# Performance work log

Measured on AMD Instinct MI355X. Metric: run time of the kernel, lower is better.

## Reference

```python
import jax, jax.numpy as jnp
import numpy as np

N, E, O, C, D_IN, OUT, L, B = 10000, 80000, 10, 64, 16, 16, 2, 16
DEG, WIDEN, BD = 3, 4, 64
EPS = 1e-6


def fibonacci_sphere(n):
    # deterministic near-uniform grid of n unit vectors on S^2 (stands in for GridGenerator's repulsion grid)
    i = jnp.arange(n, dtype=jnp.float32) + 0.5
    phi = jnp.arccos(1.0 - 2.0 * i / n)
    theta = jnp.pi * (1.0 + 5.0 ** 0.5) * i
    return jnp.stack([jnp.cos(theta) * jnp.sin(phi), jnp.sin(theta) * jnp.sin(phi), jnp.cos(phi)], axis=-1)


def poly_features(x, degree):
    # PolynomialFeatures: concat x, x(x)x, x(x)x(x)x, ... flattened outer products
    feats = [x]
    cur = x
    for _ in range(degree):
        cur = (cur[..., :, None] * x[..., None, :]).reshape(x.shape[:-1] + (-1,))
        feats.append(cur)
    return jnp.concatenate(feats, axis=-1)


def layer_norm(x, scale, bias):
    mu = jnp.mean(x, axis=-1, keepdims=True)
    var = jnp.mean((x - mu) ** 2, axis=-1, keepdims=True)
    return (x - mu) * jax.lax.rsqrt(var + EPS) * scale + bias


def setup_inputs():
    key = jax.random.key(0)
    ks = jax.random.split(key, 16)
    def w(k, shape):
        return jax.random.normal(k, shape, dtype=jnp.float32) / np.sqrt(shape[-2])
    P_SP = 2 + 4 + 8 + 16  # poly features of 2-dim spatial invariants, degree 3
    P_OR = 4               # poly features of 1-dim orientation invariant, degree 3
    return {
        "x": jax.random.normal(ks[0], (N, D_IN), jnp.float32),
        "pos": jax.random.normal(ks[1], (N, 3), jnp.float32),
        "basis_w1": w(ks[2], (P_SP, C)), "basis_b1": jnp.zeros((C,), jnp.float32),
        "basis_w2": w(ks[3], (C, BD)), "basis_b2": jnp.zeros((BD,), jnp.float32),
        "fbasis_w1": w(ks[4], (P_OR, C)), "fbasis_b1": jnp.zeros((C,), jnp.float32),
        "fbasis_w2": w(ks[5], (C, BD)), "fbasis_b2": jnp.zeros((BD,), jnp.float32),
        "embed_w": w(ks[6], (D_IN, C)),
        "conv_kw": w(ks[7], (L, BD, C)),
        "conv_fw": w(ks[8], (L, BD, C)),
        "conv_b": jnp.zeros((L, C), jnp.float32),
        "norm_s": jnp.ones((L, C), jnp.float32),
        "norm_b": jnp.zeros((L, C), jnp.float32),
        "lin1_w": w(ks[9], (L, C, WIDEN * C)), "lin1_b": jnp.zeros((L, WIDEN * C), jnp.float32),
        "lin2_w": w(ks[10], (L, WIDEN * C, C)), "lin2_b": jnp.zeros((L, C), jnp.float32),
        "ro_w": w(ks[11], (L, C, OUT)), "ro_b": jnp.zeros((L, OUT), jnp.float32),
        "edge_index": jax.random.randint(ks[12], (2, E), 0, N, jnp.int32),
        "batch": jnp.sort(jax.random.randint(ks[13], (N,), 0, B, jnp.int32)),
    }


def reference(x, pos, basis_w1, basis_b1, basis_w2, basis_b2, fbasis_w1, fbasis_b1, fbasis_w2, fbasis_b2, embed_w, conv_kw, conv_fw, conv_b, norm_s, norm_b, lin1_w, lin1_b, lin2_w, lin2_b, ro_w, ro_b, edge_index, batch):
    ori = fibonacci_sphere(O)                                             # [O,3]
    send, recv = edge_index[0], edge_index[1]
    rel = (pos[send] - pos[recv])[:, None, :]                              # [E,1,3]
    inv1 = jnp.sum(rel * ori[None], axis=-1, keepdims=True)                # [E,O,1]
    inv2 = jnp.linalg.norm(rel - inv1 * ori[None], axis=-1, keepdims=True) # [E,O,1]
    inv3 = jnp.sum(ori[None, :, :] * ori[:, None, :], axis=-1, keepdims=True)  # [O,O,1]
    sp = jnp.concatenate([inv1, inv2], axis=-1)                            # [E,O,2]
    kb = jax.nn.gelu(poly_features(sp, DEG) @ basis_w1 + basis_b1)
    kb = jax.nn.gelu(kb @ basis_w2 + basis_b2)                             # [E,O,BD]
    fkb = jax.nn.gelu(poly_features(inv3, DEG) @ fbasis_w1 + fbasis_b1)
    fkb = jax.nn.gelu(fkb @ fbasis_w2 + fbasis_b2)                         # [O,O,BD]
    h = jnp.broadcast_to((x @ embed_w)[:, None, :], (N, O, C))             # [N,O,C]
    readout = jnp.zeros((N, O, OUT), h.dtype)
    for l in range(L):
        # depthwise spatial conv: gather-send, modulate by kernel, scatter-add to receivers
        msg = h[send] * (kb @ conv_kw[l])                                  # [E,O,C]
        h1 = jax.ops.segment_sum(msg, recv, num_segments=N)                # [N,O,C]
        # depthwise fiber (orientation) conv
        fk = fkb @ conv_fw[l]                                              # [O,O,C]
        h2 = jnp.einsum('noc,poc->npc', h1, fk) / O + conv_b[l]
        # ConvNeXt MLP + residual
        y = layer_norm(h2, norm_s[l], norm_b[l])
        y = jax.nn.gelu(y @ lin1_w[l] + lin1_b[l]) @ lin2_w[l] + lin2_b[l]
        h = h + y
        readout = readout + (h @ ro_w[l] + ro_b[l])
    readout = readout / L
    out_scalar = jnp.mean(readout, axis=-2)                                # [N,OUT]
    pooled = jnp.zeros((B, OUT), out_scalar.dtype).at[batch].add(out_scalar)
    return pooled
```

## Files before the change

kernel.cpp:

```cpp
#include <hip/hip_runtime.h>
#include <math.h>

#define N_   10000
#define E_   80000
#define O_   10
#define B_   16
#define OUT_ 16
#define NROW_ (N_*O_)
#define NITEM_ (E_*O_)

typedef __attribute__((ext_vector_type(8))) short bf16x8;
typedef __attribute__((ext_vector_type(4))) short bf16x4;
typedef __attribute__((ext_vector_type(4))) float f32x4;

#define MFMA16(a,b,c) __builtin_amdgcn_mfma_f32_16x16x32_bf16(a,b,c,0,0,0)

__device__ __forceinline__ float gelu_f(float x) {
    float u = fmaf(0.044715f, x * x, 1.0f);
    float e = __builtin_amdgcn_exp2f(2.3022083f * x * u);
    float r = __builtin_amdgcn_rcpf(e + 1.0f);
    return fmaf(-x, r, x);
}

__device__ __forceinline__ unsigned short f2bf(float f) {
    union { float f; unsigned int u; } v; v.f = f;
    unsigned int r = v.u + 0x7FFFu + ((v.u >> 16) & 1u);
    return (unsigned short)(r >> 16);
}
__device__ __forceinline__ float bf2f(unsigned short u) {
    union { unsigned int u; float f; } v; v.u = ((unsigned int)u) << 16;
    return v.f;
}
__device__ __forceinline__ unsigned int cvtpk(float lo, float hi) {
    unsigned int r;
    asm("v_cvt_pk_bf16_f32 %0, %1, %2" : "=v"(r) : "v"(lo), "v"(hi));
    return r;
}
__device__ __forceinline__ bf16x4 pack4(float a, float b, float c, float d) {
    union { unsigned int u[2]; bf16x4 v; } z;
    z.u[0] = cvtpk(a, b);
    z.u[1] = cvtpk(c, d);
    return z.v;
}

__global__ __launch_bounds__(256) void k_small(
    const float* __restrict__ bw1,
    const float* __restrict__ fw1, const float* __restrict__ fb1,
    const float* __restrict__ fw2, const float* __restrict__ fb2,
    const float* __restrict__ cfw,
    const float* __restrict__ bw2, const float* __restrict__ ckw,
    const float* __restrict__ l1w, const float* __restrict__ l2w,
    const float* __restrict__ row_w,
    float* __restrict__ orig, float* __restrict__ fkg,
    unsigned short* __restrict__ wW1P, unsigned short* __restrict__ wW2P,
    unsigned short* __restrict__ wCKP, unsigned short* __restrict__ wL1P,
    unsigned short* __restrict__ wL2P, unsigned short* __restrict__ wROP)
{
    __shared__ float sOri[32];
    __shared__ float sHid[6400];
    __shared__ float sFkb[6400];
    __shared__ float sW1f[14*64];
    int tid = threadIdx.x;
    if (tid < O_) {
        float i = (float)tid + 0.5f;
        float phi = acosf(1.0f - 2.0f * i / (float)O_);
        float theta = 3.14159265358979323846f * (1.0f + 2.2360679774997896964f) * i;
        float sp = sinf(phi);
        float v0 = cosf(theta) * sp, v1 = sinf(theta) * sp, v2 = cosf(phi);
        sOri[tid*3+0] = v0; sOri[tid*3+1] = v1; sOri[tid*3+2] = v2;
        orig[tid*3+0] = v0; orig[tid*3+1] = v1; orig[tid*3+2] = v2;
    }
    {
        const int map[30] = {0,1, 2,3,3,4, 5,6,6,7,6,7,7,8,
                             9,10,10,11,10,11,11,12, 10,11,11,12, 11,12,12,13};
        for (int idx = tid; idx < 14*64; idx += 256) {
            int mono = idx >> 6, c = idx & 63;
            float s = 0.0f;
            for (int p = 0; p < 30; ++p) if (map[p] == mono) s += bw1[p*64 + c];
            sW1f[idx] = s;
        }
    }
    __syncthreads();
    for (int idx = tid; idx < 4*512; idx += 256) {
        int t = idx >> 9, rem = idx & 511;
        int ln = rem >> 3, j = rem & 7;
        int row = t*16 + (ln & 15);
        int k = (ln >> 4)*8 + j;
        wW1P[idx] = f2bf(k < 14 ? sW1f[k*64 + row] : 0.0f);
    }
    for (int idx = tid; idx < 8*512; idx += 256) {
        int t = idx >> 9, rem = idx & 511;
        int mt = t >> 1, ks = t & 1;
        int ln = rem >> 3, j = rem & 7;
        int row = mt*16 + (ln & 15);
        int k = ks*32 + (ln >> 4)*8 + j;
        wW2P[idx] = f2bf(bw2[k*64 + row]);
    }
    for (int idx = tid; idx < 2*8*512; idx += 256) {
        int l = idx >> 12, r2 = idx & 4095;
        int t = r2 >> 9, rem = r2 & 511;
        int mt = t >> 1, ks = t & 1;
        int ln = rem >> 3, j = rem & 7;
        int row = mt*16 + (ln & 15);
        int k = ks*32 + (ln >> 4)*8 + j;
        wCKP[idx] = f2bf(ckw[l*4096 + k*64 + row]);
    }
    for (int idx = tid; idx < 2*32*512; idx += 256) {
        int l = idx >> 14, r2 = idx & 16383;
        int t = r2 >> 9, rem = r2 & 511;
        int mt = t >> 1, ks = t & 1;
        int ln = rem >> 3, j = rem & 7;
        int row = mt*16 + (ln & 15);
        int k = ks*32 + (ln >> 4)*8 + j;
        wL1P[idx] = f2bf(l1w[l*16384 + k*256 + row]);
    }
    for (int idx = tid; idx < 2*32*512; idx += 256) {
        int l = idx >> 14, r2 = idx & 16383;
        int t = r2 >> 9, rem = r2 & 511;
        int mt2 = t >> 3, ksg = t & 7;
        int ln = rem >> 3, j = rem & 7;
        int row = mt2*16 + (ln & 15);
        int k = ksg*32 + (ln >> 4)*8 + j;
        wL2P[idx] = f2bf(l2w[l*16384 + k*64 + row]);
    }
    for (int idx = tid; idx < 2*2*512; idx += 256) {
        int l = idx >> 10, r2 = idx & 1023;
        int ks = r2 >> 9, rem = r2 & 511;
        int ln = rem >> 3, j = rem & 7;
        int row = ln & 15;
        int k = ks*32 + (ln >> 4)*8 + j;
        wROP[idx] = f2bf(row_w[l*1024 + k*16 + row]);
    }
    for (int it = tid; it < 6400; it += 256) {
        int pr = it >> 6, c = it & 63;
        int i = pr / O_, j = pr % O_;
        float a = sOri[i*3+0]*sOri[j*3+0] + sOri[i*3+1]*sOri[j*3+1] + sOri[i*3+2]*sOri[j*3+2];
        float f1 = a, f2 = a*a, f3 = f2*a, f4 = f3*a;
        float v = fb1[c];
        v = fmaf(f1, fw1[0*64+c], v);
        v = fmaf(f2, fw1[1*64+c], v);
        v = fmaf(f3, fw1[2*64+c], v);
        v = fmaf(f4, fw1[3*64+c], v);
        sHid[it] = gelu_f(v);
    }
    __syncthreads();
    for (int it = tid; it < 6400; it += 256) {
        int pr = it >> 6, c = it & 63;
        float v = fb2[c];
        for (int b = 0; b < 64; ++b) v = fmaf(sHid[pr*64+b], fw2[b*64+c], v);
        sFkb[it] = gelu_f(v);
    }
    __syncthreads();
    for (int l = 0; l < 2; ++l)
        for (int it = tid; it < 6400; it += 256) {
            int pr = it >> 6, c = it & 63;
            float v = 0.0f;
            for (int b = 0; b < 64; ++b) v = fmaf(sFkb[pr*64+b], cfw[l*4096 + b*64 + c], v);
            fkg[l*6400 + it] = v;
        }
}

__global__ __launch_bounds__(256) void k_embed(
    const float* __restrict__ x, const float* __restrict__ ew,
    float* __restrict__ hg, unsigned short* __restrict__ hbf0)
{
    int t = blockIdx.x * 256 + threadIdx.x;
    if (t >= N_ * 64) return;
    int n = t >> 6, c = t & 63;
    float v = 0.0f;
#pragma unroll
    for (int k = 0; k < 16; ++k) v = fmaf(x[n*16+k], ew[k*64+c], v);
    int base = n * 640 + c;
#pragma unroll
    for (int o = 0; o < O_; ++o) hg[base + o*64] = v;
    hbf0[t] = f2bf(v);
}

__global__ __launch_bounds__(256) void k_hist(const int* __restrict__ ei, int* __restrict__ counts)
{
    int e = blockIdx.x * 256 + threadIdx.x;
    if (e < E_) atomicAdd(&counts[ei[E_ + e]], 1);
}

__global__ __launch_bounds__(1024) void k_scan(
    const int* __restrict__ counts, int* __restrict__ offs, int* __restrict__ cursor)
{
    __shared__ int part[1024];
    int t = threadIdx.x;
    const int CH = 10;
    int base_i = t * CH;
    int s = 0;
#pragma unroll
    for (int i = 0; i < CH; ++i) { int idx = base_i + i; if (idx < N_) s += counts[idx]; }
    part[t] = s;
    __syncthreads();
    for (int off = 1; off < 1024; off <<= 1) {
        int v = (t >= off) ? part[t - off] : 0;
        __syncthreads();
        part[t] += v;
        __syncthreads();
    }
    int run = (t > 0) ? part[t - 1] : 0;
#pragma unroll
    for (int i = 0; i < CH; ++i) {
        int idx = base_i + i;
        if (idx < N_) { offs[idx] = run; cursor[idx] = run; run += counts[idx]; }
    }
    if (t == 1023) offs[N_] = run;
}

__global__ __launch_bounds__(256) void k_scatter(
    const int* __restrict__ ei, const float* __restrict__ pos,
    int* __restrict__ cursor, int* __restrict__ csend, int* __restrict__ crecv,
    float* __restrict__ crel)
{
    int e = blockIdx.x * 256 + threadIdx.x;
    if (e >= E_) return;
    int s = ei[e], r = ei[E_ + e];
    int slot = atomicAdd(&cursor[r], 1);
    csend[slot] = s;
    crecv[slot] = r;
    crel[slot*3+0] = pos[s*3+0] - pos[r*3+0];
    crel[slot*3+1] = pos[s*3+1] - pos[r*3+1];
    crel[slot*3+2] = pos[s*3+2] - pos[r*3+2];
}

template<int KS, bool BIAS, bool GELU>
__device__ __forceinline__ void mfma_stageP(
    unsigned short* sData, const unsigned short* __restrict__ Wp,
    const float* __restrict__ bias, int rbase, int lane)
{
    const int lm = lane & 15, lk = lane >> 4;
    bf16x8 Bf[4][KS];
#pragma unroll
    for (int nt = 0; nt < 4; ++nt)
#pragma unroll
        for (int ks = 0; ks < KS; ++ks) {
            int r = rbase + nt*16 + lm;
            int kb = ks*64 + lk*16;
            Bf[nt][ks] = *(const bf16x8*)((const char*)sData + r*128 + (kb ^ ((r&7)<<4)));
        }
#pragma unroll
    for (int mt = 0; mt < 4; ++mt) {
        bf16x8 Af[KS];
#pragma unroll
        for (int ks = 0; ks < KS; ++ks)
            Af[ks] = *(const bf16x8*)(Wp + ((mt*KS + ks)*64 + lane)*8);
        f32x4 b4 = {0,0,0,0};
        if (BIAS) b4 = *(const f32x4*)(bias + mt*16 + (lk<<2));
#pragma unroll
        for (int nt = 0; nt < 4; ++nt) {
            f32x4 acc = b4;
#pragma unroll
            for (int ks = 0; ks < KS; ++ks) acc = MFMA16(Af[ks], Bf[nt][ks], acc);
            float v0 = acc[0], v1 = acc[1], v2 = acc[2], v3 = acc[3];
            if (GELU) { v0 = gelu_f(v0); v1 = gelu_f(v1); v2 = gelu_f(v2); v3 = gelu_f(v3); }
            bf16x4 pk = pack4(v0, v1, v2, v3);
            int rr = rbase + nt*16 + lm;
            int cb = mt*32 + (lk<<3);
            *(bf16x4*)((char*)sData + rr*128 + (cb ^ ((rr&7)<<4))) = pk;
        }
    }
}

template<bool L0>
__global__ __launch_bounds__(128) void k_msg(
    const unsigned short* __restrict__ hbf, float* __restrict__ h1g,
    const int* __restrict__ csend, const int* __restrict__ crecv,
    const float* __restrict__ crel, const float* __restrict__ ori,
    const unsigned short* __restrict__ wW1P, const unsigned short* __restrict__ wW2P,
    const unsigned short* __restrict__ wCKP_l,
    const float* __restrict__ bb1, const float* __restrict__ bb2)
{
    __shared__ unsigned short sData[128*64];
    const int tid = threadIdx.x;
    const int lane = tid & 63, wv = tid >> 6;
    const int item = blockIdx.x * 128 + tid;
    const int slot = item / 10;
    const int oo = item - slot * 10;
    const int snd = csend[slot];
    const int rcv = crecv[slot];
    {
        float r0 = crel[slot*3+0], r1 = crel[slot*3+1], r2 = crel[slot*3+2];
        float o0 = ori[oo*3+0], o1 = ori[oo*3+1], o2 = ori[oo*3+2];
        float a = r0*o0 + r1*o1 + r2*o2;
        float p0 = fmaf(-a, o0, r0), p1 = fmaf(-a, o1, r1), p2 = fmaf(-a, o2, r2);
        float b = sqrtf(p0*p0 + p1*p1 + p2*p2);
        float a2 = a*a, b2 = b*b, ab = a*b;
        float m[14];
        m[0]=a; m[1]=b; m[2]=a2; m[3]=ab; m[4]=b2;
        m[5]=a2*a; m[6]=a2*b; m[7]=a*b2; m[8]=b2*b;
        m[9]=a2*a2; m[10]=a2*ab; m[11]=a2*b2; m[12]=ab*b2; m[13]=b2*b2;
        unsigned int pk[16];
#pragma unroll
        for (int j = 0; j < 7; ++j) pk[j] = cvtpk(m[2*j], m[2*j+1]);
#pragma unroll
        for (int j = 7; j < 16; ++j) pk[j] = 0;
        int r = tid;
#pragma unroll
        for (int q = 0; q < 4; ++q) {
            int cb = q*16;
            *(f32x4*)((char*)sData + r*128 + (cb ^ ((r&7)<<4))) = ((const f32x4*)pk)[q];
        }
    }
    const int rbase = wv * 64;
    mfma_stageP<1, true,  true >(sData, wW1P,   bb1, rbase, lane);
    mfma_stageP<2, true,  true >(sData, wW2P,   bb2, rbase, lane);
    mfma_stageP<2, false, false>(sData, wCKP_l, (const float*)0, rbase, lane);

    const int myaddr = L0 ? (snd * 64) : ((snd * 10 + oo) * 64);
    int prevr = __shfl_up(rcv, 1);
    unsigned long long bmask = __ballot(lane > 0 && rcv != prevr);
    const unsigned short* hb = hbf + lane;
    float a0=0,a1c=0,a2c=0,a3c=0,a4c=0,a5c=0,a6c=0,a7c=0,a8c=0,a9c=0;
    int cur = __builtin_amdgcn_readfirstlane(rcv);
    int soi = (blockIdx.x * 128 + rbase) % 10;
#define FLUSH_RUN(R) { float* bp = h1g + (R)*640 + lane; \
    atomicAdd(bp+0,a0); atomicAdd(bp+64,a1c); atomicAdd(bp+128,a2c); atomicAdd(bp+192,a3c); \
    atomicAdd(bp+256,a4c); atomicAdd(bp+320,a5c); atomicAdd(bp+384,a6c); atomicAdd(bp+448,a7c); \
    atomicAdd(bp+512,a8c); atomicAdd(bp+576,a9c); \
    a0=a1c=a2c=a3c=a4c=a5c=a6c=a7c=a8c=a9c=0.0f; }
#pragma unroll
    for (int ch = 0; ch < 4; ++ch) {
        unsigned short hvu[16];
        float kcv[16];
#pragma unroll
        for (int j = 0; j < 16; ++j) {
            const int i = ch*16 + j;
            hvu[j] = hb[__builtin_amdgcn_readlane(myaddr, i)];
            const int rr = rbase + i;
            kcv[j] = bf2f(*(const unsigned short*)((const char*)sData + rr*128 + ((lane*2) ^ ((rr&7)<<4))));
        }
#pragma unroll
        for (int j = 0; j < 16; ++j) {
            const int i = ch*16 + j;
            if (bmask & (1ull << i)) { FLUSH_RUN(cur); cur = __builtin_amdgcn_readlane(rcv, i); }
            float mv = kcv[j] * bf2f(hvu[j]);
            if      (soi == 0) a0  += mv;
            else if (soi == 1) a1c += mv;
            else if (soi == 2) a2c += mv;
            else if (soi == 3) a3c += mv;
            else if (soi == 4) a4c += mv;
            else if (soi == 5) a5c += mv;
            else if (soi == 6) a6c += mv;
            else if (soi == 7) a7c += mv;
            else if (soi == 8) a8c += mv;
            else               a9c += mv;
            soi = (soi == 9) ? 0 : soi + 1;
        }
    }
    FLUSH_RUN(cur);
#undef FLUSH_RUN
}

__global__ __launch_bounds__(256) void k_fln(
    const float* __restrict__ h1, const float* __restrict__ fkg,
    const float* __restrict__ cb, const float* __restrict__ ns,
    const float* __restrict__ nb, unsigned short* __restrict__ y)
{
    __shared__ float sFK[6400];
    const int tid = threadIdx.x;
    for (int i = tid; i < 6400; i += 256) sFK[i] = fkg[i];
    __syncthreads();
    const int lane = tid & 63, wv = tid >> 6;
    float cbv = cb[lane], nsv = ns[lane], nbv = nb[lane];
    for (int g4 = blockIdx.x; g4 < N_/4; g4 += gridDim.x) {
        const int n = g4 * 4 + wv;
        float hr[10];
#pragma unroll
        for (int o = 0; o < O_; ++o) hr[o] = h1[n*640 + o*64 + lane];
#pragma unroll
        for (int p = 0; p < O_; ++p) {
            float v = 0.0f;
#pragma unroll
            for (int o = 0; o < O_; ++o) v = fmaf(hr[o], sFK[(p*O_+o)*64 + lane], v);
            v = v * 0.1f + cbv;
            float s = v, q = v*v;
#pragma unroll
            for (int d = 1; d < 64; d <<= 1) { s += __shfl_xor(s, d); q += __shfl_xor(q, d); }
            float mu = s * (1.0f/64.0f);
            float var = q * (1.0f/64.0f) - mu*mu;
            float rs = rsqrtf(var + 1e-6f);
            float yv = (v - mu) * rs * nsv + nbv;
            y[(n*O_ + p)*64 + lane] = f2bf(yv);
        }
    }
}

__global__ __launch_bounds__(256, 4) void k_mlp(
    unsigned short* ybuf, float* __restrict__ hg, float* __restrict__ rout,
    const unsigned short* __restrict__ wL1P_l, const float* __restrict__ l1b_l,
    const unsigned short* __restrict__ wL2P_l, const float* __restrict__ l2b_l,
    const unsigned short* __restrict__ wROP_l, const float* __restrict__ rob_l)
{
    __shared__ unsigned short sA[64*64];
    const int tid = threadIdx.x;
    const int lane = tid & 63, wv = tid >> 6;
    const int rb = blockIdx.x * 64;
#pragma unroll
    for (int i = tid*16; i < 64*128; i += 256*16) {
        int r = i >> 7, off = i & 127;
        int grow = rb + r; if (grow >= NROW_) grow = NROW_ - 1;
        *(f32x4*)((char*)sA + r*128 + (off ^ ((r&7)<<4))) =
            *(const f32x4*)((const char*)ybuf + (size_t)grow*128 + off);
    }
    __syncthreads();
    const int lm = lane & 15, lk = lane >> 4;
    const int r0 = wv*16 + lm;
    bf16x8 Yf[2];
#pragma unroll
    for (int ks = 0; ks < 2; ++ks) {
        int kb = ks*64 + lk*16;
        Yf[ks] = *(const bf16x8*)((const char*)sA + r0*128 + (kb ^ ((r0&7)<<4)));
    }
    f32x4 acc2[4];
#pragma unroll
    for (int m = 0; m < 4; ++m) acc2[m] = *(const f32x4*)(l2b_l + m*16 + (lk<<2));
#pragma unroll
    for (int jb = 0; jb < 4; ++jb) {
#pragma unroll
        for (int mt = 0; mt < 4; ++mt) {
            bf16x8 A1[2];
#pragma unroll
            for (int ks = 0; ks < 2; ++ks)
                A1[ks] = *(const bf16x8*)(wL1P_l + (((jb*4 + mt)*2 + ks)*64 + lane)*8);
            f32x4 acc = *(const f32x4*)(l1b_l + jb*64 + mt*16 + (lk<<2));
            acc = MFMA16(A1[0], Yf[0], acc);
            acc = MFMA16(A1[1], Yf[1], acc);
            bf16x4 pk = pack4(gelu_f(acc[0]), gelu_f(acc[1]), gelu_f(acc[2]), gelu_f(acc[3]));
            int cb = mt*32 + (lk<<3);
            *(bf16x4*)((char*)sA + r0*128 + (cb ^ ((r0&7)<<4))) = pk;
        }
        bf16x8 Mf[2];
#pragma unroll
        for (int ks = 0; ks < 2; ++ks) {
            int kb = ks*64 + lk*16;
            Mf[ks] = *(const bf16x8*)((const char*)sA + r0*128 + (kb ^ ((r0&7)<<4)));
        }
#pragma unroll
        for (int mt2 = 0; mt2 < 4; ++mt2) {
            bf16x8 A2[2];
#pragma unroll
            for (int ks = 0; ks < 2; ++ks)
                A2[ks] = *(const bf16x8*)(wL2P_l + ((mt2*8 + jb*2 + ks)*64 + lane)*8);
            acc2[mt2] = MFMA16(A2[0], Mf[0], acc2[mt2]);
            acc2[mt2] = MFMA16(A2[1], Mf[1], acc2[mt2]);
        }
    }
    const int grow = rb + r0;
    const bool valid = grow < NROW_;
    const int growc = valid ? grow : (NROW_ - 1);
#pragma unroll
    for (int mt2 = 0; mt2 < 4; ++mt2) {
        f32x4 hv = *(const f32x4*)(hg + (size_t)growc*64 + mt2*16 + (lk<<2));
        f32x4 hn;
#pragma unroll
        for (int r = 0; r < 4; ++r) hn[r] = hv[r] + acc2[mt2][r];
        bf16x4 pk = pack4(hn[0], hn[1], hn[2], hn[3]);
        if (valid) {
            *(f32x4*)(hg + (size_t)grow*64 + mt2*16 + (lk<<2)) = hn;
            *(bf16x4*)((char*)ybuf + (size_t)grow*128 + (mt2*16 + (lk<<2))*2) = pk;
        }
        int cb = mt2*32 + (lk<<3);
        *(bf16x4*)((char*)sA + r0*128 + (cb ^ ((r0&7)<<4))) = pk;
    }
    bf16x8 Ro[2];
#pragma unroll
    for (int ks = 0; ks < 2; ++ks)
        Ro[ks] = *(const bf16x8*)(wROP_l + (ks*64 + lane)*8);
    f32x4 r4 = *(const f32x4*)(rob_l + (lk<<2));
    bf16x8 Hf[2];
#pragma unroll
    for (int ks = 0; ks < 2; ++ks) {
        int kb = ks*64 + lk*16;
        Hf[ks] = *(const bf16x8*)((const char*)sA + r0*128 + (kb ^ ((r0&7)<<4)));
    }
    r4 = MFMA16(Ro[0], Hf[0], r4);
    r4 = MFMA16(Ro[1], Hf[1], r4);
    if (valid) *(f32x4*)(rout + (size_t)grow*16 + (lk<<2)) = r4;
}

__global__ __launch_bounds__(256) void k_pool(
    const float* __restrict__ r0, const float* __restrict__ r1,
    const int* __restrict__ batch, float* __restrict__ out)
{
    int t = blockIdx.x * 256 + threadIdx.x;
    if (t >= N_ * 16) return;
    int n = t >> 4, j = t & 15;
    float s = 0.0f;
#pragma unroll
    for (int p = 0; p < O_; ++p)
        s += r0[(n*O_ + p)*16 + j] + r1[(n*O_ + p)*16 + j];
    atomicAdd(&out[batch[n]*16 + j], s * (1.0f/20.0f));
}

extern "C" void kernel_launch(void* const* d_in, const int* in_sizes, int n_in,
                              void* d_out, int out_size, void* d_ws, size_t ws_size,
                              hipStream_t stream)
{
    const float* x    = (const float*)d_in[0];
    const float* pos  = (const float*)d_in[1];
    const float* bw1  = (const float*)d_in[2];
    const float* bb1  = (const float*)d_in[3];
    const float* bw2  = (const float*)d_in[4];
    const float* bb2  = (const float*)d_in[5];
    const float* fw1  = (const float*)d_in[6];
    const float* fb1  = (const float*)d_in[7];
    const float* fw2  = (const float*)d_in[8];
    const float* fb2  = (const float*)d_in[9];
    const float* embw = (const float*)d_in[10];
    const float* ckw  = (const float*)d_in[11];
    const float* cfw  = (const float*)d_in[12];
    const float* cb   = (const float*)d_in[13];
    const float* ns   = (const float*)d_in[14];
    const float* nbp  = (const float*)d_in[15];
    const float* l1w  = (const float*)d_in[16];
    const float* l1b  = (const float*)d_in[17];
    const float* l2w  = (const float*)d_in[18];
    const float* l2b  = (const float*)d_in[19];
    const float* row  = (const float*)d_in[20];
    const float* rob  = (const float*)d_in[21];
    const int*   ei   = (const int*)d_in[22];
    const int*   batch= (const int*)d_in[23];
    float* out = (float*)d_out;

    char* w = (char*)d_ws;
    size_t off = 0;
    auto alloc = [&](size_t bytes) -> char* {
        char* p = w + off; off += (bytes + 255) / 256 * 256; return p;
    };
    float* ori    = (float*)alloc(32 * 4);
    float* fkg    = (float*)alloc(2 * 6400 * 4);
    unsigned short* wW1P = (unsigned short*)alloc(4*512*2);
    unsigned short* wW2P = (unsigned short*)alloc(8*512*2);
    unsigned short* wCKP = (unsigned short*)alloc(2*8*512*2);
    unsigned short* wL1P = (unsigned short*)alloc(2*32*512*2);
    unsigned short* wL2P = (unsigned short*)alloc(2*32*512*2);
    unsigned short* wROP = (unsigned short*)alloc(2*2*512*2);
    float* h      = (float*)alloc((size_t)N_ * 640 * 4);
    float* h1     = (float*)alloc((size_t)N_ * 640 * 4);
    unsigned short* y = (unsigned short*)alloc((size_t)NROW_ * 64 * 2);
    unsigned short* hbf0 = (unsigned short*)alloc((size_t)N_ * 64 * 2);
    float* rout0  = (float*)alloc((size_t)NROW_ * 16 * 4);
    float* rout1  = (float*)alloc((size_t)NROW_ * 16 * 4);
    float* crel   = (float*)alloc((size_t)E_ * 3 * 4);
    int*   counts = (int*)alloc((N_ + 1) * 4);
    int*   offs   = (int*)alloc((N_ + 1) * 4);
    int*   cursor = (int*)alloc((N_ + 1) * 4);
    int*   csend  = (int*)alloc((size_t)E_ * 4);
    int*   crecv  = (int*)alloc((size_t)E_ * 4);

    hipMemsetAsync(out, 0, (size_t)out_size * 4, stream);
    hipMemsetAsync(counts, 0, (N_ + 1) * 4, stream);

    k_small<<<1, 256, 0, stream>>>(bw1, fw1, fb1, fw2, fb2, cfw, bw2, ckw, l1w, l2w, row,
                                   ori, fkg, wW1P, wW2P, wCKP, wL1P, wL2P, wROP);
    k_embed<<<(N_ * 64 + 255) / 256, 256, 0, stream>>>(x, embw, h, hbf0);
    k_hist<<<(E_ + 255) / 256, 256, 0, stream>>>(ei, counts);
    k_scan<<<1, 1024, 0, stream>>>(counts, offs, cursor);
    k_scatter<<<(E_ + 255) / 256, 256, 0, stream>>>(ei, pos, cursor, csend, crecv, crel);

    for (int l = 0; l < 2; ++l) {
        hipMemsetAsync(h1, 0, (size_t)N_ * 640 * 4, stream);
        if (l == 0)
            k_msg<true><<<NITEM_ / 128, 128, 0, stream>>>(hbf0, h1, csend, crecv, crel, ori,
                                                          wW1P, wW2P, wCKP + l*4096, bb1, bb2);
        else
            k_msg<false><<<NITEM_ / 128, 128, 0, stream>>>(y, h1, csend, crecv, crel, ori,
                                                           wW1P, wW2P, wCKP + l*4096, bb1, bb2);
        k_fln<<<625, 256, 0, stream>>>(h1, fkg + l*6400, cb + l*64, ns + l*64, nbp + l*64, y);
        k_mlp<<<(NROW_ + 63) / 64, 256, 0, stream>>>(y, h, (l == 0 ? rout0 : rout1),
                                                     wL1P + l*16384, l1b + l*256,
                                                     wL2P + l*16384, l2b + l*64,
                                                     wROP + l*1024, rob + l*16);
    }
    k_pool<<<(N_ * 16 + 255) / 256, 256, 0, stream>>>(rout0, rout1, batch, out);
}
```

Baseline: 478.6 us.

## Split single-block weight-prep kernel into grid-parallel pack and fiber-basis kernels

The old setup kernel ran as a single 256-thread block that serially packed all weights into bf16 MFMA layouts and computed the fiber-basis MLP and conv kernels. It is replaced by a 321-block packing kernel, with one thread per packed element, and a separate 25-block kernel where each wavefront computes one orientation pair's MLP row. The aim is to remove a long serial prologue that occupied one CU while the rest of the GPU sat idle. It adds one extra launch, and each pair now recomputes its Fibonacci vectors.

```diff
diff --git a/kernel.cpp b/kernel.cpp
--- a/kernel.cpp
+++ b/kernel.cpp
@@ -43,60 +43,49 @@
     return z.v;
 }
 
-__global__ __launch_bounds__(256) void k_small(
-    const float* __restrict__ bw1,
-    const float* __restrict__ fw1, const float* __restrict__ fb1,
-    const float* __restrict__ fw2, const float* __restrict__ fb2,
-    const float* __restrict__ cfw,
-    const float* __restrict__ bw2, const float* __restrict__ ckw,
-    const float* __restrict__ l1w, const float* __restrict__ l2w,
-    const float* __restrict__ row_w,
-    float* __restrict__ orig, float* __restrict__ fkg,
+__device__ __forceinline__ void fib_vec(int idx, float& vx, float& vy, float& vz) {
+    float i = (float)idx + 0.5f;
+    float phi = acosf(1.0f - 2.0f * i / (float)O_);
+    float theta = 3.14159265358979323846f * (1.0f + 2.2360679774997896964f) * i;
+    float sp = sinf(phi);
+    vx = cosf(theta) * sp; vy = sinf(theta) * sp; vz = cosf(phi);
+}
+
+__global__ __launch_bounds__(256) void k_pack(
+    const float* __restrict__ bw1, const float* __restrict__ bw2,
+    const float* __restrict__ ckw, const float* __restrict__ l1w,
+    const float* __restrict__ l2w, const float* __restrict__ row_w,
+    float* __restrict__ orig,
     unsigned short* __restrict__ wW1P, unsigned short* __restrict__ wW2P,
     unsigned short* __restrict__ wCKP, unsigned short* __restrict__ wL1P,
     unsigned short* __restrict__ wL2P, unsigned short* __restrict__ wROP)
 {
-    __shared__ float sOri[32];
-    __shared__ float sHid[6400];
-    __shared__ float sFkb[6400];
-    __shared__ float sW1f[14*64];
-    int tid = threadIdx.x;
-    if (tid < O_) {
-        float i = (float)tid + 0.5f;
-        float phi = acosf(1.0f - 2.0f * i / (float)O_);
-        float theta = 3.14159265358979323846f * (1.0f + 2.2360679774997896964f) * i;
-        float sp = sinf(phi);
-        float v0 = cosf(theta) * sp, v1 = sinf(theta) * sp, v2 = cosf(phi);
-        sOri[tid*3+0] = v0; sOri[tid*3+1] = v1; sOri[tid*3+2] = v2;
-        orig[tid*3+0] = v0; orig[tid*3+1] = v1; orig[tid*3+2] = v2;
-    }
-    {
-        const int map[30] = {0,1, 2,3,3,4, 5,6,6,7,6,7,7,8,
-                             9,10,10,11,10,11,11,12, 10,11,11,12, 11,12,12,13};
-        for (int idx = tid; idx < 14*64; idx += 256) {
-            int mono = idx >> 6, c = idx & 63;
-            float s = 0.0f;
-            for (int p = 0; p < 30; ++p) if (map[p] == mono) s += bw1[p*64 + c];
-            sW1f[idx] = s;
-        }
-    }
-    __syncthreads();
-    for (int idx = tid; idx < 4*512; idx += 256) {
+    const int g = blockIdx.x * 256 + threadIdx.x;
+    if (g < 2048) {
+        int idx = g;
         int t = idx >> 9, rem = idx & 511;
         int ln = rem >> 3, j = rem & 7;
         int row = t*16 + (ln & 15);
         int k = (ln >> 4)*8 + j;
-        wW1P[idx] = f2bf(k < 14 ? sW1f[k*64 + row] : 0.0f);
-    }
-    for (int idx = tid; idx < 8*512; idx += 256) {
+        float s = 0.0f;
+        if (k < 14) {
+            const int moff[14] = {0,1,2,3,5,6,7,10,13,14,15,19,25,29};
+            const int mcnt[14] = {1,1,1,2,1,1,3,3,1,1,4,6,4,1};
+            const int mlist[30] = {0,1,2,3,4,5,6,7,8,10,9,11,12,13,14,
+                                   15,16,18,22,17,19,20,23,24,26,21,25,27,28,29};
+            for (int q = 0; q < mcnt[k]; ++q) s += bw1[mlist[moff[k]+q]*64 + row];
+        }
+        wW1P[idx] = f2bf(s);
+    } else if (g < 6144) {
+        int idx = g - 2048;
         int t = idx >> 9, rem = idx & 511;
         int mt = t >> 1, ks = t & 1;
         int ln = rem >> 3, j = rem & 7;
         int row = mt*16 + (ln & 15);
         int k = ks*32 + (ln >> 4)*8 + j;
         wW2P[idx] = f2bf(bw2[k*64 + row]);
-    }
-    for (int idx = tid; idx < 2*8*512; idx += 256) {
+    } else if (g < 14336) {
+        int idx = g - 6144;
         int l = idx >> 12, r2 = idx & 4095;
         int t = r2 >> 9, rem = r2 & 511;
         int mt = t >> 1, ks = t & 1;
@@ -104,8 +93,8 @@
         int row = mt*16 + (ln & 15);
         int k = ks*32 + (ln >> 4)*8 + j;
         wCKP[idx] = f2bf(ckw[l*4096 + k*64 + row]);
-    }
-    for (int idx = tid; idx < 2*32*512; idx += 256) {
+    } else if (g < 47104) {
+        int idx = g - 14336;
         int l = idx >> 14, r2 = idx & 16383;
         int t = r2 >> 9, rem = r2 & 511;
         int mt = t >> 1, ks = t & 1;
@@ -113,8 +102,8 @@
         int row = mt*16 + (ln & 15);
         int k = ks*32 + (ln >> 4)*8 + j;
         wL1P[idx] = f2bf(l1w[l*16384 + k*256 + row]);
-    }
-    for (int idx = tid; idx < 2*32*512; idx += 256) {
+    } else if (g < 79872) {
+        int idx = g - 47104;
         int l = idx >> 14, r2 = idx & 16383;
         int t = r2 >> 9, rem = r2 & 511;
         int mt2 = t >> 3, ksg = t & 7;
@@ -122,42 +111,51 @@
         int row = mt2*16 + (ln & 15);
         int k = ksg*32 + (ln >> 4)*8 + j;
         wL2P[idx] = f2bf(l2w[l*16384 + k*64 + row]);
-    }
-    for (int idx = tid; idx < 2*2*512; idx += 256) {
+    } else if (g < 81920) {
+        int idx = g - 79872;
         int l = idx >> 10, r2 = idx & 1023;
         int ks = r2 >> 9, rem = r2 & 511;
         int ln = rem >> 3, j = rem & 7;
         int row = ln & 15;
         int k = ks*32 + (ln >> 4)*8 + j;
         wROP[idx] = f2bf(row_w[l*1024 + k*16 + row]);
-    }
-    for (int it = tid; it < 6400; it += 256) {
-        int pr = it >> 6, c = it & 63;
-        int i = pr / O_, j = pr % O_;
-        float a = sOri[i*3+0]*sOri[j*3+0] + sOri[i*3+1]*sOri[j*3+1] + sOri[i*3+2]*sOri[j*3+2];
-        float f1 = a, f2 = a*a, f3 = f2*a, f4 = f3*a;
-        float v = fb1[c];
-        v = fmaf(f1, fw1[0*64+c], v);
-        v = fmaf(f2, fw1[1*64+c], v);
-        v = fmaf(f3, fw1[2*64+c], v);
-        v = fmaf(f4, fw1[3*64+c], v);
-        sHid[it] = gelu_f(v);
-    }
-    __syncthreads();
-    for (int it = tid; it < 6400; it += 256) {
-        int pr = it >> 6, c = it & 63;
-        float v = fb2[c];
-        for (int b = 0; b < 64; ++b) v = fmaf(sHid[pr*64+b], fw2[b*64+c], v);
-        sFkb[it] = gelu_f(v);
-    }
-    __syncthreads();
-    for (int l = 0; l < 2; ++l)
-        for (int it = tid; it < 6400; it += 256) {
-            int pr = it >> 6, c = it & 63;
-            float v = 0.0f;
-            for (int b = 0; b < 64; ++b) v = fmaf(sFkb[pr*64+b], cfw[l*4096 + b*64 + c], v);
-            fkg[l*6400 + it] = v;
-        }
+    } else if (g < 81920 + O_) {
+        int o = g - 81920;
+        float vx, vy, vz;
+        fib_vec(o, vx, vy, vz);
+        orig[o*3+0] = vx; orig[o*3+1] = vy; orig[o*3+2] = vz;
+    }
+}
+
+__global__ __launch_bounds__(256) void k_fibpre(
+    const float* __restrict__ fw1, const float* __restrict__ fb1,
+    const float* __restrict__ fw2, const float* __restrict__ fb2,
+    const float* __restrict__ cfw, float* __restrict__ fkg)
+{
+    __shared__ float sRow[4][64];
+    const int wv = threadIdx.x >> 6, lane = threadIdx.x & 63;
+    const int pr = blockIdx.x * 4 + wv;
+    if (pr >= 100) return;
+    const int i = pr / O_, j = pr % O_;
+    float ix, iy, iz, jx, jy, jz;
+    fib_vec(i, ix, iy, iz);
+    fib_vec(j, jx, jy, jz);
+    float a = ix*jx + iy*jy + iz*jz;
+    float a2 = a*a, a3 = a2*a, a4 = a3*a;
+    float v = fb1[lane];
+    v = fmaf(a,  fw1[0*64+lane], v);
+    v = fmaf(a2, fw1[1*64+lane], v);
+    v = fmaf(a3, fw1[2*64+lane], v);
+    v = fmaf(a4, fw1[3*64+lane], v);
+    sRow[wv][lane] = gelu_f(v);
+    float acc = fb2[lane];
+    for (int b = 0; b < 64; ++b) acc = fmaf(sRow[wv][b], fw2[b*64+lane], acc);
+    sRow[wv][lane] = gelu_f(acc);
+    for (int l = 0; l < 2; ++l) {
+        float s = 0.0f;
+        for (int b = 0; b < 64; ++b) s = fmaf(sRow[wv][b], cfw[l*4096 + b*64 + lane], s);
+        fkg[l*6400 + pr*64 + lane] = s;
+    }
 }
 
 __global__ __launch_bounds__(256) void k_embed(
@@ -553,8 +551,9 @@
     hipMemsetAsync(out, 0, (size_t)out_size * 4, stream);
     hipMemsetAsync(counts, 0, (N_ + 1) * 4, stream);
 
-    k_small<<<1, 256, 0, stream>>>(bw1, fw1, fb1, fw2, fb2, cfw, bw2, ckw, l1w, l2w, row,
-                                   ori, fkg, wW1P, wW2P, wCKP, wL1P, wL2P, wROP);
+    k_pack<<<321, 256, 0, stream>>>(bw1, bw2, ckw, l1w, l2w, row, ori,
+                                    wW1P, wW2P, wCKP, wL1P, wL2P, wROP);
+    k_fibpre<<<25, 256, 0, stream>>>(fw1, fb1, fw2, fb2, cfw, fkg);
     k_embed<<<(N_ * 64 + 255) / 256, 256, 0, stream>>>(x, embw, h, hbf0);
     k_hist<<<(E_ + 255) / 256, 256, 0, stream>>>(ei, counts);
     k_scan<<<1, 1024, 0, stream>>>(counts, offs, cursor);
```

Result: faster. 432.7 us (-9.6%).
